# Performance work log

Measured on AMD Instinct MI355X. Metric: run time of the kernel, lower is better.

## Reference

```python
import jax, jax.numpy as jnp
import numpy as np

NUM_HEADS = 16
DIM = 1024
HD = DIM // NUM_HEADS  # 64


def setup_inputs() -> dict:
    key = jax.random.key(0)
    ks = jax.random.split(key, 7)
    B, S = 4, 2048
    def xavier(k, shape, fan_in, fan_out):
        bound = float(np.sqrt(6.0 / (fan_in + fan_out)))
        return jax.random.uniform(k, shape, jnp.float32, -bound, bound)
    return {
        "q": jax.random.normal(ks[0], (B, S, DIM), jnp.float32),
        "k": jax.random.normal(ks[1], (B, S, DIM), jnp.float32),
        "v": jax.random.normal(ks[2], (B, S, DIM), jnp.float32),
        "Wq": xavier(ks[3], (NUM_HEADS, DIM, HD), DIM, HD),
        "Wk": xavier(ks[4], (NUM_HEADS, DIM, HD), DIM, HD),
        "Wv": xavier(ks[5], (NUM_HEADS, DIM, HD), DIM, HD),
        "Wo": xavier(ks[6], (DIM, DIM), DIM, DIM),
    }


def reference(q, k, v, Wq, Wk, Wv, Wo):
    B, S, D = q.shape
    norm = jnp.sqrt(jnp.asarray(HD, q.dtype))
    # per-head projections: [B,S,D] x [H,D,hd] -> [B,H,S,hd]
    qh = jnp.einsum('bsd,hde->bhse', q, Wq)
    kh = jnp.einsum('bsd,hde->bhse', k, Wk)
    vh = jnp.einsum('bsd,hde->bhse', v, Wv)
    # scores [B,H,S,S]
    scores = jnp.einsum('bhse,bhte->bhst', qh, kh) / norm
    causal = jnp.triu(jnp.ones((S, S), bool), k=1)
    scores = jnp.where(causal, -jnp.inf, scores)
    attn = jax.nn.softmax(scores, axis=-1)
    out = jnp.einsum('bhst,bhte->bhse', attn, vh)  # [B,H,S,hd]
    # faithful to original: a raw view of [B,H,S,hd] -> [B,S,H*hd] (no head transpose)
    out = out.reshape(B, S, NUM_HEADS * HD)
    return jnp.matmul(out, Wo)
```

## Files before the change

kernel.cpp:

```cpp
#include <hip/hip_runtime.h>
#include <hip/hip_bf16.h>
#include <stdint.h>

typedef __bf16 bf16;
typedef __bf16 bf16x8 __attribute__((ext_vector_type(8)));
typedef __bf16 bf16x4 __attribute__((ext_vector_type(4)));
typedef __bf16 bf16x2 __attribute__((ext_vector_type(2)));
typedef float f32x4 __attribute__((ext_vector_type(4)));
typedef float f32x16 __attribute__((ext_vector_type(16)));
typedef int i32x4 __attribute__((ext_vector_type(4)));

#define NH   16
#define SEQ  2048
#define DM   1024
#define HD   64
#define THRD 11.0f

__device__ __forceinline__ int swz(int r, int o) {
  return o ^ ((r & 7) << 4) ^ (((r >> 3) & 1) << 5);
}

__device__ __forceinline__ void gll16(const void* g, void* l) {
  __builtin_amdgcn_global_load_lds(
      (__attribute__((address_space(1))) unsigned int*)(g),
      (__attribute__((address_space(3))) unsigned int*)(l), 16, 0, 0);
}

__device__ __forceinline__ int pk2(float a, float b) {
  bf16x2 t; t[0] = (bf16)a; t[1] = (bf16)b;
  return __builtin_bit_cast(int, t);
}

__global__ __launch_bounds__(256) void conv_wt(const float* __restrict__ Wq,
                                               const float* __restrict__ Wk,
                                               const float* __restrict__ Wv,
                                               const float* __restrict__ Wo,
                                               bf16* __restrict__ WqT,
                                               bf16* __restrict__ WkT,
                                               bf16* __restrict__ WvT,
                                               bf16* __restrict__ WoT) {
  __shared__ float tile[64][65];
  int z = blockIdx.z, t = threadIdx.x;
  int d0 = blockIdx.x << 6;
  if (z < 3) {
    const float* W = (z == 0 ? Wq : z == 1 ? Wk : Wv) + ((size_t)blockIdx.y << 16);
#pragma unroll
    for (int i = 0; i < 4; ++i) {
      int slot = (i << 8) + t;
      int r = slot >> 4, c4 = (slot & 15) << 2;
      float4 fv = *(const float4*)(W + (size_t)(d0 + r) * 64 + c4);
      tile[r][c4] = fv.x; tile[r][c4 + 1] = fv.y;
      tile[r][c4 + 2] = fv.z; tile[r][c4 + 3] = fv.w;
    }
  } else {
    int n0 = blockIdx.y << 6;
#pragma unroll
    for (int i = 0; i < 4; ++i) {
      int slot = (i << 8) + t;
      int r = slot >> 4, c4 = (slot & 15) << 2;
      float4 fv = *(const float4*)(Wo + (size_t)(d0 + r) * 1024 + n0 + c4);
      tile[r][c4] = fv.x; tile[r][c4 + 1] = fv.y;
      tile[r][c4 + 2] = fv.z; tile[r][c4 + 3] = fv.w;
    }
  }
  __syncthreads();
  bf16* Wt = z == 0 ? WqT : z == 1 ? WkT : z == 2 ? WvT : WoT;
  size_t base = (z < 3) ? ((size_t)blockIdx.y << 16)
                        : (size_t)(blockIdx.y << 6) * 1024;
  int e = t >> 2, dq = (t & 3) << 4;
  bf16x8 o0, o1;
#pragma unroll
  for (int j = 0; j < 8; ++j) {
    o0[j] = (bf16)tile[dq + j][e];
    o1[j] = (bf16)tile[dq + 8 + j][e];
  }
  bf16* p = Wt + base + (size_t)e * 1024 + d0 + dq;
  *(bf16x8*)p = o0;
  *(bf16x8*)(p + 8) = o1;
}

__global__ __launch_bounds__(256) void conv_one(const float* __restrict__ src,
                                                bf16* __restrict__ dst) {
  int i = (blockIdx.x * 256 + threadIdx.x) << 2;
  float4 f = *(const float4*)(src + i);
  bf16x4 o; o[0] = (bf16)f.x; o[1] = (bf16)f.y; o[2] = (bf16)f.z; o[3] = (bf16)f.w;
  *(bf16x4*)(dst + i) = o;
}

__global__ __launch_bounds__(256, 2) void gemm_bt16(const bf16* __restrict__ A,
                                                    const bf16* __restrict__ Bt,
                                                    void* __restrict__ Cv,
                                                    int epi, float scale) {
  __shared__ char sm[32768];
  char* As = sm;
  char* Bs = sm + 16384;
  int tid = threadIdx.x;
  int wid = tid >> 6, lane = tid & 63;
  int g = lane >> 4, cc = lane & 15;
  int wr = wid >> 1, wc = wid & 1;
  int n0 = blockIdx.x << 7;
  int m0 = blockIdx.y << 7;

  f32x4 acc[4][4];
#pragma unroll
  for (int a = 0; a < 4; ++a)
#pragma unroll
    for (int b = 0; b < 4; ++b)
#pragma unroll
      for (int j = 0; j < 4; ++j) acc[a][b][j] = 0.0f;

  for (int kt = 0; kt < 16; ++kt) {
    int k0 = kt << 6;
#pragma unroll
    for (int it = 0; it < 4; ++it) {
      int L = (it << 12) + (tid << 4);
      int r = L >> 7, o = L & 127;
      int os = swz(r, o);
      gll16(Bt + (size_t)(n0 + r) * 1024 + k0 + (os >> 1),
            Bs + (it << 12) + (wid << 10));
      gll16(A + (size_t)(m0 + r) * 1024 + k0 + (os >> 1),
            As + (it << 12) + (wid << 10));
    }
    __syncthreads();
#pragma unroll
    for (int kk = 0; kk < 2; ++kk) {
      bf16x8 af[4], bfr[4];
#pragma unroll
      for (int fm = 0; fm < 4; ++fm) {
        int r = (wr << 6) + (fm << 4) + cc;
        af[fm] = *(const bf16x8*)(As + (r << 7) + swz(r, (kk << 6) + (g << 4)));
      }
#pragma unroll
      for (int fn = 0; fn < 4; ++fn) {
        int r = (wc << 6) + (fn << 4) + cc;
        bfr[fn] = *(const bf16x8*)(Bs + (r << 7) + swz(r, (kk << 6) + (g << 4)));
      }
#pragma unroll
      for (int fm = 0; fm < 4; ++fm)
#pragma unroll
        for (int fn = 0; fn < 4; ++fn)
          acc[fm][fn] = __builtin_amdgcn_mfma_f32_16x16x32_bf16(
              af[fm], bfr[fn], acc[fm][fn], 0, 0, 0);
    }
    __syncthreads();
  }

#pragma unroll
  for (int fm = 0; fm < 4; ++fm) {
#pragma unroll
    for (int fn = 0; fn < 4; ++fn) {
      f32x4 v = acc[fm][fn];
      int mr = m0 + (wr << 6) + (fm << 4) + (g << 2);
      int n = n0 + (wc << 6) + (fn << 4) + cc;
      if (epi == 2) {
        float* C = (float*)Cv;
#pragma unroll
        for (int j = 0; j < 4; ++j) C[(size_t)(mr + j) * 1024 + n] = v[j];
      } else if (epi == 0) {
        bf16* C = (bf16*)Cv;
        int h = n >> 6, e = n & 63;
#pragma unroll
        for (int j = 0; j < 4; ++j) {
          int b = (mr + j) >> 11, s = (mr + j) & 2047;
          C[((size_t)(b * NH + h) * SEQ + s) * HD + e] = (bf16)(v[j] * scale);
        }
      } else {
        bf16* C = (bf16*)Cv;
        int h = n >> 6, e = n & 63;
        int b = mr >> 11, s = mr & 2047;
        bf16x4 t;
#pragma unroll
        for (int j = 0; j < 4; ++j) t[j] = (bf16)v[j];
        *(bf16x4*)(C + ((size_t)(b * NH + h) * HD + e) * SEQ + s) = t;
      }
    }
  }
}

__global__ __launch_bounds__(256, 3) void attn_fwd(const bf16* __restrict__ Qh,
                                                   const bf16* __restrict__ Kh,
                                                   const bf16* __restrict__ Vt,
                                                   bf16* __restrict__ Oa) {
  __shared__ char sm[32768];
  int tid = threadIdx.x, wid = tid >> 6;
  int lane = tid & 63, cc = lane & 31, hi = lane >> 5;
  int h4 = hi << 2;
  int qp = blockIdx.x, bh = blockIdx.y;
  const bf16* Kb = Kh + (size_t)bh * SEQ * HD;
  const bf16* Vb = Vt + (size_t)bh * HD * SEQ;

  for (int ph = 0; ph < 2; ++ph) {
    int qx = ph ? (15 - qp) : qp;
    int q0 = qx << 7;
    int sb = q0 + (wid << 5);

    const bf16* Qp = Qh + ((size_t)bh * SEQ + sb + cc) * HD + (hi << 3);
    bf16x8 qf[4];
#pragma unroll
    for (int kk = 0; kk < 4; ++kk) qf[kk] = *(const bf16x8*)(Qp + (kk << 4));

    f32x16 acc[2];
#pragma unroll
    for (int eb = 0; eb < 2; ++eb)
#pragma unroll
      for (int r = 0; r < 16; ++r) acc[eb][r] = 0.f;
    float m = -3e38f, l = 0.f;

    int nkv = (qx << 1) + 2;
    int cur = 0;
#pragma unroll
    for (int i2 = 0; i2 < 2; ++i2) {
      int L = (i2 << 12) + (tid << 4);
      int r = L >> 7, o = L & 127;
      int os = swz(r, o);
      gll16(Kb + (size_t)r * HD + (os >> 1), sm + (i2 << 12) + (wid << 10));
      gll16(Vb + (size_t)r * SEQ + (os >> 1), sm + 8192 + (i2 << 12) + (wid << 10));
    }
    asm volatile("s_waitcnt vmcnt(0)" ::: "memory");
    __builtin_amdgcn_s_barrier();
    __builtin_amdgcn_sched_barrier(0);

    for (int it = 0; it < nkv; ++it) {
      int t0 = it << 6;
      char* Ks = sm + (cur << 14);
      char* Vs = Ks + 8192;
      if (it + 1 < nkv) {
        char* nb = sm + ((cur ^ 1) << 14);
        int t1 = t0 + 64;
#pragma unroll
        for (int i2 = 0; i2 < 2; ++i2) {
          int L = (i2 << 12) + (tid << 4);
          int r = L >> 7, o = L & 127;
          int os = swz(r, o);
          gll16(Kb + (size_t)(t1 + r) * HD + (os >> 1),
                nb + (i2 << 12) + (wid << 10));
          gll16(Vb + (size_t)r * SEQ + t1 + (os >> 1),
                nb + 8192 + (i2 << 12) + (wid << 10));
        }
      }
      if (t0 <= sb + 31) {
        f32x16 sc[2];
#pragma unroll
        for (int tb = 0; tb < 2; ++tb) {
#pragma unroll
          for (int r = 0; r < 16; ++r) sc[tb][r] = 0.f;
#pragma unroll
          for (int kk = 0; kk < 4; ++kk) {
            int rr = (tb << 5) + cc;
            bf16x8 kf = *(const bf16x8*)(Ks + (rr << 7) +
                                         swz(rr, (kk << 5) + (hi << 4)));
            sc[tb] = __builtin_amdgcn_mfma_f32_32x32x16_bf16(kf, qf[kk],
                                                             sc[tb], 0, 0, 0);
          }
        }
        if (t0 + 63 > sb) {
          int s = sb + cc;
#pragma unroll
          for (int tb = 0; tb < 2; ++tb)
#pragma unroll
            for (int r = 0; r < 16; ++r) {
              int t = t0 + (tb << 5) + (r & 3) + ((r >> 2) << 3) + h4;
              if (t > s) sc[tb][r] = -3e38f;
            }
        }
        float tm[16];
#pragma unroll
        for (int r = 0; r < 16; ++r) tm[r] = fmaxf(sc[0][r], sc[1][r]);
#pragma unroll
        for (int s2 = 8; s2 >= 1; s2 >>= 1)
#pragma unroll
          for (int r = 0; r < 8; ++r)
            if (r < s2) tm[r] = fmaxf(tm[r], tm[r + s2]);
        float pm = fmaxf(tm[0], __shfl_xor(tm[0], 32, 64));
        if (!__all(pm - m <= THRD)) {
          float mn = fmaxf(m, pm);
          float sclf = exp2f(m - mn);
          m = mn; l *= sclf;
          int sclb = __builtin_bit_cast(int, sclf);
#pragma unroll
          for (int r = 0; r < 16; ++r) {
            int ssel = (r & 3) + ((r >> 2) << 3) + h4;
            float sr = __builtin_bit_cast(
                float, __builtin_amdgcn_ds_bpermute(ssel << 2, sclb));
            acc[0][r] *= sr;
            acc[1][r] *= sr;
          }
        }
        float ts[16];
#pragma unroll
        for (int r = 0; r < 16; ++r) {
          float p0 = exp2f(sc[0][r] - m);
          float p1 = exp2f(sc[1][r] - m);
          sc[0][r] = p0; sc[1][r] = p1;
          ts[r] = p0 + p1;
        }
#pragma unroll
        for (int s2 = 8; s2 >= 1; s2 >>= 1)
#pragma unroll
          for (int r = 0; r < 8; ++r)
            if (r < s2) ts[r] += ts[r + s2];
        l += ts[0] + __shfl_xor(ts[0], 32, 64);
#pragma unroll
        for (int ks = 0; ks < 4; ++ks) {
          int tb = ks >> 1, base = (ks & 1) << 3;
          int w00 = pk2(sc[tb][base + 0], sc[tb][base + 1]);
          int w01 = pk2(sc[tb][base + 2], sc[tb][base + 3]);
          int w10 = pk2(sc[tb][base + 4], sc[tb][base + 5]);
          int w11 = pk2(sc[tb][base + 6], sc[tb][base + 7]);
          int selB0 = hi ? w00 : w10;
          int selB1 = hi ? w01 : w11;
          int cross0 = __shfl_xor(selB0, 32, 64);
          int cross1 = __shfl_xor(selB1, 32, 64);
          i32x4 wv;
          wv[0] = hi ? cross0 : w00;
          wv[1] = hi ? cross1 : w01;
          wv[2] = hi ? w10 : cross0;
          wv[3] = hi ? w11 : cross1;
          bf16x8 pa = __builtin_bit_cast(bf16x8, wv);
#pragma unroll
          for (int eb = 0; eb < 2; ++eb) {
            int rr = (eb << 5) + cc;
            bf16x8 vf = *(const bf16x8*)(Vs + (rr << 7) +
                                         swz(rr, (ks << 5) + (hi << 4)));
            acc[eb] = __builtin_amdgcn_mfma_f32_32x32x16_bf16(pa, vf,
                                                              acc[eb], 0, 0, 0);
          }
        }
      }
      asm volatile("s_waitcnt vmcnt(0)" ::: "memory");
      __builtin_amdgcn_s_barrier();
      __builtin_amdgcn_sched_barrier(0);
      cur ^= 1;
    }
    float invl = 1.0f / l;
    int ilb = __builtin_bit_cast(int, invl);
    bf16* Op = Oa + ((size_t)bh * SEQ + sb) * HD;
#pragma unroll
    for (int r = 0; r < 16; ++r) {
      int ssel = (r & 3) + ((r >> 2) << 3) + h4;
      float ir = __builtin_bit_cast(
          float, __builtin_amdgcn_ds_bpermute(ssel << 2, ilb));
#pragma unroll
      for (int eb = 0; eb < 2; ++eb)
        Op[(size_t)ssel * HD + (eb << 5) + cc] = (bf16)(acc[eb][r] * ir);
    }
  }
}

extern "C" void kernel_launch(void* const* d_in, const int* in_sizes, int n_in,
                              void* d_out, int out_size, void* d_ws,
                              size_t ws_size, hipStream_t stream) {
  const float* q = (const float*)d_in[0];
  const float* k = (const float*)d_in[1];
  const float* v = (const float*)d_in[2];
  const float* Wq = (const float*)d_in[3];
  const float* Wk = (const float*)d_in[4];
  const float* Wv = (const float*)d_in[5];
  const float* Wo = (const float*)d_in[6];
  char* ws = (char*)d_ws;

  const size_t MB = 1024 * 1024;
  const float qscale = 0.125f * 1.44269504f;

  bf16* WqT = (bf16*)(ws + 0 * MB);
  bf16* WkT = (bf16*)(ws + 2 * MB);
  bf16* WvT = (bf16*)(ws + 4 * MB);
  bf16* WoT = (bf16*)(ws + 6 * MB);
  bf16* tmp = (bf16*)(ws + 8 * MB);
  bf16* Qh  = (bf16*)(ws + 24 * MB);
  bf16* Kh  = (bf16*)(ws + 40 * MB);
  bf16* Vt  = (bf16*)(ws + 56 * MB);
  bf16* Att = tmp;

  conv_wt<<<dim3(16, 16, 4), 256, 0, stream>>>(Wq, Wk, Wv, Wo,
                                               WqT, WkT, WvT, WoT);

  dim3 gg(8, 64);
  conv_one<<<8192, 256, 0, stream>>>(q, tmp);
  gemm_bt16<<<gg, 256, 0, stream>>>(tmp, WqT, Qh, 0, qscale);
  conv_one<<<8192, 256, 0, stream>>>(k, tmp);
  gemm_bt16<<<gg, 256, 0, stream>>>(tmp, WkT, Kh, 0, 1.0f);
  conv_one<<<8192, 256, 0, stream>>>(v, tmp);
  gemm_bt16<<<gg, 256, 0, stream>>>(tmp, WvT, Vt, 1, 1.0f);

  attn_fwd<<<dim3(8, 64), 256, 0, stream>>>(Qh, Kh, Vt, Att);

  gemm_bt16<<<gg, 256, 0, stream>>>(Att, WoT, (float*)d_out, 2, 1.0f);
}
```

Baseline: 222.4 us.

## Fuse fp32-to-bf16 input conversion into batched QKV GEMM and remap blocks across XCDs

Drops the three separate conversion kernels and fuses fp32-to-bf16 conversion of q/k/v into the GEMM A-tile load. The three projection GEMMs now run as a single launch with z selecting q, k or v. A block-index remap groups blocks that share B tiles or heads onto the same XCD for L2 reuse, and it is applied to the GEMMs and to attention. This removes the bf16 intermediate write/read and several launches. In exchange, the A-tile load now goes through registers with synchronous loads and no direct-to-LDS path, which may add latency inside the GEMM.

```diff
diff --git a/kernel.cpp b/kernel.cpp
--- a/kernel.cpp
+++ b/kernel.cpp
@@ -29,6 +29,11 @@
 __device__ __forceinline__ int pk2(float a, float b) {
   bf16x2 t; t[0] = (bf16)a; t[1] = (bf16)b;
   return __builtin_bit_cast(int, t);
+}
+
+__device__ __forceinline__ void xcd_remap(int& tx, int& ty) {
+  tx = blockIdx.y & 7;
+  ty = ((int)blockIdx.x << 3) + ((int)blockIdx.y >> 3);
 }
 
 __global__ __launch_bounds__(256) void conv_wt(const float* __restrict__ Wq,
@@ -79,27 +84,16 @@
   *(bf16x8*)(p + 8) = o1;
 }
 
-__global__ __launch_bounds__(256) void conv_one(const float* __restrict__ src,
-                                                bf16* __restrict__ dst) {
-  int i = (blockIdx.x * 256 + threadIdx.x) << 2;
-  float4 f = *(const float4*)(src + i);
-  bf16x4 o; o[0] = (bf16)f.x; o[1] = (bf16)f.y; o[2] = (bf16)f.z; o[3] = (bf16)f.w;
-  *(bf16x4*)(dst + i) = o;
-}
-
-__global__ __launch_bounds__(256, 2) void gemm_bt16(const bf16* __restrict__ A,
-                                                    const bf16* __restrict__ Bt,
-                                                    void* __restrict__ Cv,
-                                                    int epi, float scale) {
-  __shared__ char sm[32768];
+template <bool AF32>
+__device__ __forceinline__ void gemm_body(char* sm, const void* Av,
+                                          const bf16* Bt, void* Cv, int epi,
+                                          float scale, int n0, int m0) {
   char* As = sm;
   char* Bs = sm + 16384;
   int tid = threadIdx.x;
   int wid = tid >> 6, lane = tid & 63;
   int g = lane >> 4, cc = lane & 15;
   int wr = wid >> 1, wc = wid & 1;
-  int n0 = blockIdx.x << 7;
-  int m0 = blockIdx.y << 7;
 
   f32x4 acc[4][4];
 #pragma unroll
@@ -118,8 +112,32 @@
       int os = swz(r, o);
       gll16(Bt + (size_t)(n0 + r) * 1024 + k0 + (os >> 1),
             Bs + (it << 12) + (wid << 10));
-      gll16(A + (size_t)(m0 + r) * 1024 + k0 + (os >> 1),
-            As + (it << 12) + (wid << 10));
+    }
+    if constexpr (AF32) {
+      const float* A = (const float*)Av;
+      int r = tid >> 1, hf = tid & 1;
+      const float* src = A + (size_t)(m0 + r) * 1024 + k0 + hf * 32;
+      float4 fv[8];
+#pragma unroll
+      for (int q = 0; q < 8; ++q) fv[q] = ((const float4*)src)[q];
+#pragma unroll
+      for (int q = 0; q < 4; ++q) {
+        float4 a = fv[2 * q], b = fv[2 * q + 1];
+        bf16x8 pk;
+        pk[0] = (bf16)a.x; pk[1] = (bf16)a.y; pk[2] = (bf16)a.z; pk[3] = (bf16)a.w;
+        pk[4] = (bf16)b.x; pk[5] = (bf16)b.y; pk[6] = (bf16)b.z; pk[7] = (bf16)b.w;
+        *(bf16x8*)(As + (r << 7) + swz(r, hf * 64 + q * 16)) = pk;
+      }
+    } else {
+      const bf16* A = (const bf16*)Av;
+#pragma unroll
+      for (int it = 0; it < 4; ++it) {
+        int L = (it << 12) + (tid << 4);
+        int r = L >> 7, o = L & 127;
+        int os = swz(r, o);
+        gll16(A + (size_t)(m0 + r) * 1024 + k0 + (os >> 1),
+              As + (it << 12) + (wid << 10));
+      }
     }
     __syncthreads();
 #pragma unroll
@@ -175,6 +193,32 @@
       }
     }
   }
+}
+
+__global__ __launch_bounds__(256, 2) void gemm_qkv_f32(
+    const float* __restrict__ q, const float* __restrict__ k,
+    const float* __restrict__ v, const bf16* __restrict__ Wq,
+    const bf16* __restrict__ Wk, const bf16* __restrict__ Wv,
+    bf16* __restrict__ Qh, bf16* __restrict__ Kh, bf16* __restrict__ Vt,
+    float qscale) {
+  __shared__ char sm[32768];
+  int z = blockIdx.z;
+  const void* A = z == 0 ? (const void*)q : z == 1 ? (const void*)k : (const void*)v;
+  const bf16* B = z == 0 ? Wq : z == 1 ? Wk : Wv;
+  void* C = z == 0 ? (void*)Qh : z == 1 ? (void*)Kh : (void*)Vt;
+  int tx, ty;
+  xcd_remap(tx, ty);
+  gemm_body<true>(sm, A, B, C, z == 2 ? 1 : 0, z == 0 ? qscale : 1.0f,
+                  tx << 7, ty << 7);
+}
+
+__global__ __launch_bounds__(256, 2) void gemm_o(const bf16* __restrict__ Att,
+                                                 const bf16* __restrict__ Wo,
+                                                 float* __restrict__ out) {
+  __shared__ char sm[32768];
+  int tx, ty;
+  xcd_remap(tx, ty);
+  gemm_body<false>(sm, Att, Wo, out, 2, 1.0f, tx << 7, ty << 7);
 }
 
 __global__ __launch_bounds__(256, 3) void attn_fwd(const bf16* __restrict__ Qh,
@@ -185,7 +229,8 @@
   int tid = threadIdx.x, wid = tid >> 6;
   int lane = tid & 63, cc = lane & 31, hi = lane >> 5;
   int h4 = hi << 2;
-  int qp = blockIdx.x, bh = blockIdx.y;
+  int qp, bh;
+  xcd_remap(qp, bh);
   const bf16* Kb = Kh + (size_t)bh * SEQ * HD;
   const bf16* Vb = Vt + (size_t)bh * HD * SEQ;
 
@@ -366,24 +411,18 @@
   bf16* WkT = (bf16*)(ws + 2 * MB);
   bf16* WvT = (bf16*)(ws + 4 * MB);
   bf16* WoT = (bf16*)(ws + 6 * MB);
-  bf16* tmp = (bf16*)(ws + 8 * MB);
-  bf16* Qh  = (bf16*)(ws + 24 * MB);
-  bf16* Kh  = (bf16*)(ws + 40 * MB);
-  bf16* Vt  = (bf16*)(ws + 56 * MB);
-  bf16* Att = tmp;
+  bf16* Qh  = (bf16*)(ws + 8 * MB);
+  bf16* Kh  = (bf16*)(ws + 24 * MB);
+  bf16* Vt  = (bf16*)(ws + 40 * MB);
+  bf16* Att = (bf16*)(ws + 56 * MB);
 
   conv_wt<<<dim3(16, 16, 4), 256, 0, stream>>>(Wq, Wk, Wv, Wo,
                                                WqT, WkT, WvT, WoT);
 
-  dim3 gg(8, 64);
-  conv_one<<<8192, 256, 0, stream>>>(q, tmp);
-  gemm_bt16<<<gg, 256, 0, stream>>>(tmp, WqT, Qh, 0, qscale);
-  conv_one<<<8192, 256, 0, stream>>>(k, tmp);
-  gemm_bt16<<<gg, 256, 0, stream>>>(tmp, WkT, Kh, 0, 1.0f);
-  conv_one<<<8192, 256, 0, stream>>>(v, tmp);
-  gemm_bt16<<<gg, 256, 0, stream>>>(tmp, WvT, Vt, 1, 1.0f);
+  gemm_qkv_f32<<<dim3(8, 64, 3), 256, 0, stream>>>(
+      q, k, v, WqT, WkT, WvT, Qh, Kh, Vt, qscale);
 
   attn_fwd<<<dim3(8, 64), 256, 0, stream>>>(Qh, Kh, Vt, Att);
 
-  gemm_bt16<<<gg, 256, 0, stream>>>(Att, WoT, (float*)d_out, 2, 1.0f);
-}
+  gemm_o<<<dim3(8, 64), 256, 0, stream>>>(Att, WoT, (float*)d_out);
+}
```

Result: slower. 227.3 us (+2.2%).
